# Kernel tuning notes

Hardware: AMD Instinct MI355X
Metric: run time of the kernel (lower is better)

## Reference

```python
import jax, jax.numpy as jnp
import numpy as np

TOP_K = 8
N_GROUP = 8
TOPK_GROUP = 4
ROUTED_SCALING_FACTOR = 2.5
NUM_EXPERTS = 256
HIDDEN = 7168
NUM_TOKENS = 16384


def setup_inputs() -> dict:
    key = jax.random.key(0)
    k1, k2, k3 = jax.random.split(key, 3)
    hidden_states = jax.random.normal(k1, (NUM_TOKENS, HIDDEN), dtype=jnp.float32)
    weight = jax.random.normal(k2, (NUM_EXPERTS, HIDDEN), dtype=jnp.float32) * 0.02
    e_score_correction_bias = jax.random.normal(k3, (NUM_EXPERTS,), dtype=jnp.float32) * 0.1
    return {
        "hidden_states": hidden_states,
        "weight": weight,
        "e_score_correction_bias": e_score_correction_bias,
    }


def reference(hidden_states, weight, e_score_correction_bias):
    # logits: [T, E] = hidden_states @ weight.T  (fp32 gate GEMM)
    logits = jnp.einsum("th,eh->te", hidden_states.astype(jnp.float32), weight)
    scores = jax.nn.sigmoid(logits)                      # [T, E]
    scores_with_bias = scores + e_score_correction_bias  # [T, E]
    T, E = scores_with_bias.shape
    gs = E // N_GROUP  # experts per group

    # group score = sum of top-2 biased scores within each group
    grouped = scores_with_bias.reshape(T, N_GROUP, gs)
    top2, _ = jax.lax.top_k(grouped, 2)                  # [T, G, 2]
    group_scores = top2.sum(axis=-1)                     # [T, G]

    # select topk_group groups, build group mask
    _, group_idx = jax.lax.top_k(group_scores, TOPK_GROUP)  # [T, topk_group]
    rows = jnp.arange(T)[:, None]
    group_mask = jnp.zeros_like(group_scores).at[rows, group_idx].set(1.0)  # [T, G]

    # expand group mask to experts and mask biased scores
    score_mask = jnp.repeat(group_mask, gs, axis=-1)     # [T, E]
    masked_swb = scores_with_bias * score_mask

    # top-k experts over masked biased scores; mask raw sigmoid scores
    _, topk_idx = jax.lax.top_k(masked_swb, TOP_K)       # [T, top_k]
    new_mask = jnp.zeros_like(scores).at[rows, topk_idx].set(1.0)
    sel = scores * new_mask

    # renormalize selected scores and apply routed scaling
    denom = sel.sum(axis=-1, keepdims=True) + 1e-20
    return sel / denom * ROUTED_SCALING_FACTOR
```

## Files before the change

### kernel.cpp

```cpp
#include <hip/hip_runtime.h>
#include <cstdint>
#include <cstddef>

#define HIDDEN 7168
#define NEXP   256
#define KSTEPS (HIDDEN / 32)
#define BM     64
#define ROUTED_SCALE 2.5f


typedef _Float16 half8 __attribute__((ext_vector_type(8)));
typedef float    f32x4 __attribute__((ext_vector_type(4)));

__global__ void convert_w(const float* __restrict__ w, _Float16* __restrict__ ws) {
    int e = blockIdx.x;
    int nt = e >> 4, row = e & 15;
    for (int k = threadIdx.x; k < HIDDEN; k += 256) {
        float x = w[(size_t)e * HIDDEN + k] * 64.0f;
        _Float16 hi = (_Float16)x;
        _Float16 lo = (_Float16)((x - (float)hi) * 4096.0f);
        int s = k >> 5, q = (k >> 3) & 3, j = k & 7;
        size_t off = (size_t)(q * 16 + row) * 8 + j;
        ws[((size_t)((s * 2 + 0) * 16 + nt) << 9) + off] = hi;
        ws[((size_t)((s * 2 + 1) * 16 + nt) << 9) + off] = lo;
    }
}

__global__ __launch_bounds__(512, 2) void gate_kernel(
    const float* __restrict__ hidden,
    const _Float16* __restrict__ wsB,
    const float* __restrict__ bias,
    float* __restrict__ out) {

    __shared__ float lds[BM * 256];

    const int tid    = threadIdx.x;
    const int w      = tid >> 6;
    const int wm     = w >> 2;
    const int wn     = w & 3;
    const int l      = tid & 63;
    const int lane15 = l & 15;
    const int quad   = l >> 4;
    const size_t blockRow = (size_t)blockIdx.x * BM;

    const float* A0 = hidden + (blockRow + wm * 32) * HIDDEN + quad * 8;
    const float* Ap[2];
#pragma unroll
    for (int mt = 0; mt < 2; ++mt)
        Ap[mt] = A0 + (size_t)(mt * 16 + lane15) * HIDDEN;

    const _Float16* Bl = wsB + l * 8;

    f32x4 acc_hh[2][4], acc_c1[2][4];
#pragma unroll
    for (int i = 0; i < 2; ++i)
#pragma unroll
        for (int j = 0; j < 4; ++j) {
            acc_hh[i][j] = (f32x4)0.0f;
            acc_c1[i][j] = (f32x4)0.0f;
        }

    auto loadA = [&](int s, f32x4 (&a)[2][2]) {
#pragma unroll
        for (int mt = 0; mt < 2; ++mt) {
            const float* p = Ap[mt] + s * 32;
            a[mt][0] = *(const f32x4*)(p);
            a[mt][1] = *(const f32x4*)(p + 4);
        }
    };
    auto loadB = [&](int s, half8 (&bh)[4], half8 (&bl)[4]) {
#pragma unroll
        for (int jj = 0; jj < 4; ++jj) {
            int nt = wn * 4 + jj;
            bh[jj] = *(const half8*)(Bl + ((size_t)((s * 2 + 0) * 16 + nt) << 9));
            bl[jj] = *(const half8*)(Bl + ((size_t)((s * 2 + 1) * 16 + nt) << 9));
        }
    };
    auto compute = [&](f32x4 (&a)[2][2], half8 (&bh)[4], half8 (&bl)[4]) {
        half8 ah[2], al[2];
#pragma unroll
        for (int mt = 0; mt < 2; ++mt) {
#pragma unroll
            for (int e = 0; e < 8; ++e) {
                float x = (e < 4) ? a[mt][0][e] : a[mt][1][e - 4];
                _Float16 h = (_Float16)x;
                ah[mt][e] = h;
                al[mt][e] = (_Float16)((x - (float)h) * 4096.0f);
            }
        }
#pragma unroll
        for (int jj = 0; jj < 4; ++jj)
#pragma unroll
            for (int mt = 0; mt < 2; ++mt)
                acc_hh[mt][jj] = __builtin_amdgcn_mfma_f32_16x16x32_f16(ah[mt], bh[jj], acc_hh[mt][jj], 0, 0, 0);
#pragma unroll
        for (int jj = 0; jj < 4; ++jj)
#pragma unroll
            for (int mt = 0; mt < 2; ++mt)
                acc_c1[mt][jj] = __builtin_amdgcn_mfma_f32_16x16x32_f16(al[mt], bh[jj], acc_c1[mt][jj], 0, 0, 0);
#pragma unroll
        for (int jj = 0; jj < 4; ++jj)
#pragma unroll
            for (int mt = 0; mt < 2; ++mt)
                acc_c1[mt][jj] = __builtin_amdgcn_mfma_f32_16x16x32_f16(ah[mt], bl[jj], acc_c1[mt][jj], 0, 0, 0);
    };

    f32x4 a0[2][2], a1[2][2];
    half8 bh0[4], bl0[4], bh1[4], bl1[4];

    loadA(0, a0); loadB(0, bh0, bl0);
    for (int s = 0; s < KSTEPS; s += 2) {
        loadA(s + 1, a1); loadB(s + 1, bh1, bl1);
        compute(a0, bh0, bl0);
        if (s != KSTEPS - 2) { loadA(s + 2, a0); loadB(s + 2, bh0, bl0); }
        compute(a1, bh1, bl1);
    }

#pragma unroll
    for (int mt = 0; mt < 2; ++mt)
#pragma unroll
        for (int jj = 0; jj < 4; ++jj)
#pragma unroll
            for (int r = 0; r < 4; ++r) {
                int row = wm * 32 + mt * 16 + quad * 4 + r;
                int col = wn * 64 + jj * 16 + lane15;
                float logit = (acc_hh[mt][jj][r] + acc_c1[mt][jj][r] * (1.0f / 4096.0f)) * (1.0f / 64.0f);
                lds[row * 256 + col] = logit;
            }
    __syncthreads();

    const int t = tid >> 3;
    const int p = tid & 7;
    float* Lrow = &lds[t * 256];
    const int rot = (t * 4 + p) & 31;

    float t0 = -1e30f, t1 = -1e30f;
    for (int i = 0; i < 32; ++i) {
        int col = p * 32 + ((i + rot) & 31);
        float x  = Lrow[col];
        float sg = 1.0f / (1.0f + expf(-x));
        Lrow[col] = sg;
        float swb = sg + bias[col];
        t1 = fmaxf(t1, fminf(t0, swb));
        t0 = fmaxf(t0, swb);
    }
    float gs = t0 + t1;

    int rank = 0;
#pragma unroll
    for (int m = 1; m < 8; ++m) {
        float ov = __shfl_xor(gs, m);
        int   og = p ^ m;
        rank += (int)((ov > gs) || (ov == gs && og < p));
    }
    bool sel = rank < 4;

    float lv[8], lsr[8]; int li[8];
#pragma unroll
    for (int k = 0; k < 8; ++k) { lv[k] = -1.0f; lsr[k] = 0.0f; li[k] = 1 << 30; }
    for (int i = 0; i < 32; ++i) {
        int col = p * 32 + ((i + rot) & 31);
        float sg  = Lrow[col];
        float swb = sg + bias[col];
        float v = (sel && swb > 0.0f) ? swb : -1.0f;
        if (v > lv[7]) {
            float cv = v, cs = sg; int ci = col;
#pragma unroll
            for (int k = 0; k < 8; ++k) {
                bool sw = cv > lv[k];
                float tv = lv[k], ts = lsr[k]; int ti = li[k];
                lv[k]  = sw ? cv : tv;  lsr[k] = sw ? cs : ts;  li[k] = sw ? ci : ti;
                cv = sw ? tv : cv;  cs = sw ? ts : cs;  ci = sw ? ti : ci;
            }
        }
    }

    unsigned selmask = 0u;
    float denom = 0.0f;
#pragma unroll
    for (int round = 0; round < 8; ++round) {
        float hv = lv[0], hs = lsr[0]; int hidx = li[0];
#pragma unroll
        for (int m = 1; m <= 4; m <<= 1) {
            float ov = __shfl_xor(hv, m);
            float os = __shfl_xor(hs, m);
            int   oi = __shfl_xor(hidx, m);
            bool take = (ov > hv) || (ov == hv && oi < hidx);
            hv = take ? ov : hv;  hs = take ? os : hs;  hidx = take ? oi : hidx;
        }
        if (hv > 0.0f) {
            denom += hs;
            if ((hidx >> 5) == p) selmask |= (1u << (hidx & 31));
        }
        if (li[0] == hidx) {
#pragma unroll
            for (int k = 0; k < 7; ++k) { lv[k] = lv[k + 1]; lsr[k] = lsr[k + 1]; li[k] = li[k + 1]; }
            lv[7] = -1.0f; lsr[7] = 0.0f; li[7] = 1 << 30;
        }
    }

    float inv = ROUTED_SCALE / (denom + 1e-20f);
    float* orow = out + (blockRow + (size_t)t) * NEXP;
    for (int i = 0; i < 32; i += 4) {
        int ii = (i + ((rot & 7) << 2)) & 31;
        int col = p * 32 + ii;
        f32x4 v;
#pragma unroll
        for (int u = 0; u < 4; ++u) {
            float sg = Lrow[col + u];
            bool on = (selmask >> ((col + u) & 31)) & 1u;
            v[u] = on ? sg * inv : 0.0f;
        }
        *(f32x4*)(orow + col) = v;
    }
}

extern "C" void kernel_launch(void* const* d_in, const int* in_sizes, int n_in,
                              void* d_out, int out_size, void* d_ws, size_t ws_size,
                              hipStream_t stream) {
    const float* hidden = (const float*)d_in[0];
    const float* weight = (const float*)d_in[1];
    const float* bias   = (const float*)d_in[2];
    float* out = (float*)d_out;
    _Float16* ws = (_Float16*)d_ws;

    convert_w<<<NEXP, 256, 0, stream>>>(weight, ws);
    gate_kernel<<<16384 / BM, 512, 0, stream>>>(hidden, ws, bias, out);
}
```

Before: 907.4 us.

## Halve gate GEMM row tile to 32 and raise occupancy to four blocks

Shrinks the per-block token tile from 64 to 32 rows, so each wave now computes one 16-row M tile instead of two. The launch bound becomes four blocks per CU, and only half the threads run the routing epilogue. The aim is lower register pressure and more waves in flight to hide global-memory latency on the A/B loads. In exchange, each B (weight) fragment loaded from global memory is reused by half as many MFMAs, so total weight traffic through the caches doubles.

```diff
diff --git a/kernel.cpp b/kernel.cpp
--- a/kernel.cpp
+++ b/kernel.cpp
@@ -5,7 +5,7 @@
 #define HIDDEN 7168
 #define NEXP   256
 #define KSTEPS (HIDDEN / 32)
-#define BM     64
+#define BM     32
 #define ROUTED_SCALE 2.5f
 
 
@@ -26,7 +26,7 @@
     }
 }
 
-__global__ __launch_bounds__(512, 2) void gate_kernel(
+__global__ __launch_bounds__(512, 4) void gate_kernel(
     const float* __restrict__ hidden,
     const _Float16* __restrict__ wsB,
     const float* __restrict__ bias,
@@ -43,30 +43,21 @@
     const int quad   = l >> 4;
     const size_t blockRow = (size_t)blockIdx.x * BM;
 
-    const float* A0 = hidden + (blockRow + wm * 32) * HIDDEN + quad * 8;
-    const float* Ap[2];
-#pragma unroll
-    for (int mt = 0; mt < 2; ++mt)
-        Ap[mt] = A0 + (size_t)(mt * 16 + lane15) * HIDDEN;
+    const float* Ap = hidden + (blockRow + wm * 16 + lane15) * HIDDEN + quad * 8;
 
     const _Float16* Bl = wsB + l * 8;
 
-    f32x4 acc_hh[2][4], acc_c1[2][4];
-#pragma unroll
-    for (int i = 0; i < 2; ++i)
-#pragma unroll
-        for (int j = 0; j < 4; ++j) {
-            acc_hh[i][j] = (f32x4)0.0f;
-            acc_c1[i][j] = (f32x4)0.0f;
-        }
-
-    auto loadA = [&](int s, f32x4 (&a)[2][2]) {
-#pragma unroll
-        for (int mt = 0; mt < 2; ++mt) {
-            const float* p = Ap[mt] + s * 32;
-            a[mt][0] = *(const f32x4*)(p);
-            a[mt][1] = *(const f32x4*)(p + 4);
-        }
+    f32x4 acc_hh[4], acc_c1[4];
+#pragma unroll
+    for (int j = 0; j < 4; ++j) {
+        acc_hh[j] = (f32x4)0.0f;
+        acc_c1[j] = (f32x4)0.0f;
+    }
+
+    auto loadA = [&](int s, f32x4 (&a)[2]) {
+        const float* p = Ap + s * 32;
+        a[0] = *(const f32x4*)(p);
+        a[1] = *(const f32x4*)(p + 4);
     };
     auto loadB = [&](int s, half8 (&bh)[4], half8 (&bl)[4]) {
 #pragma unroll
@@ -76,36 +67,27 @@
             bl[jj] = *(const half8*)(Bl + ((size_t)((s * 2 + 1) * 16 + nt) << 9));
         }
     };
-    auto compute = [&](f32x4 (&a)[2][2], half8 (&bh)[4], half8 (&bl)[4]) {
-        half8 ah[2], al[2];
-#pragma unroll
-        for (int mt = 0; mt < 2; ++mt) {
-#pragma unroll
-            for (int e = 0; e < 8; ++e) {
-                float x = (e < 4) ? a[mt][0][e] : a[mt][1][e - 4];
-                _Float16 h = (_Float16)x;
-                ah[mt][e] = h;
-                al[mt][e] = (_Float16)((x - (float)h) * 4096.0f);
-            }
+    auto compute = [&](f32x4 (&a)[2], half8 (&bh)[4], half8 (&bl)[4]) {
+        half8 ah, al;
+#pragma unroll
+        for (int e = 0; e < 8; ++e) {
+            float x = (e < 4) ? a[0][e] : a[1][e - 4];
+            _Float16 h = (_Float16)x;
+            ah[e] = h;
+            al[e] = (_Float16)((x - (float)h) * 4096.0f);
         }
 #pragma unroll
         for (int jj = 0; jj < 4; ++jj)
-#pragma unroll
-            for (int mt = 0; mt < 2; ++mt)
-                acc_hh[mt][jj] = __builtin_amdgcn_mfma_f32_16x16x32_f16(ah[mt], bh[jj], acc_hh[mt][jj], 0, 0, 0);
+            acc_hh[jj] = __builtin_amdgcn_mfma_f32_16x16x32_f16(ah, bh[jj], acc_hh[jj], 0, 0, 0);
 #pragma unroll
         for (int jj = 0; jj < 4; ++jj)
-#pragma unroll
-            for (int mt = 0; mt < 2; ++mt)
-                acc_c1[mt][jj] = __builtin_amdgcn_mfma_f32_16x16x32_f16(al[mt], bh[jj], acc_c1[mt][jj], 0, 0, 0);
+            acc_c1[jj] = __builtin_amdgcn_mfma_f32_16x16x32_f16(al, bh[jj], acc_c1[jj], 0, 0, 0);
 #pragma unroll
         for (int jj = 0; jj < 4; ++jj)
-#pragma unroll
-            for (int mt = 0; mt < 2; ++mt)
-                acc_c1[mt][jj] = __builtin_amdgcn_mfma_f32_16x16x32_f16(ah[mt], bl[jj], acc_c1[mt][jj], 0, 0, 0);
+            acc_c1[jj] = __builtin_amdgcn_mfma_f32_16x16x32_f16(ah, bl[jj], acc_c1[jj], 0, 0, 0);
     };
 
-    f32x4 a0[2][2], a1[2][2];
+    f32x4 a0[2], a1[2];
     half8 bh0[4], bl0[4], bh1[4], bl1[4];
 
     loadA(0, a0); loadB(0, bh0, bl0);
@@ -117,101 +99,101 @@
     }
 
 #pragma unroll
-    for (int mt = 0; mt < 2; ++mt)
-#pragma unroll
-        for (int jj = 0; jj < 4; ++jj)
-#pragma unroll
-            for (int r = 0; r < 4; ++r) {
-                int row = wm * 32 + mt * 16 + quad * 4 + r;
-                int col = wn * 64 + jj * 16 + lane15;
-                float logit = (acc_hh[mt][jj][r] + acc_c1[mt][jj][r] * (1.0f / 4096.0f)) * (1.0f / 64.0f);
-                lds[row * 256 + col] = logit;
-            }
+    for (int jj = 0; jj < 4; ++jj)
+#pragma unroll
+        for (int r = 0; r < 4; ++r) {
+            int row = wm * 16 + quad * 4 + r;
+            int col = wn * 64 + jj * 16 + lane15;
+            float logit = (acc_hh[jj][r] + acc_c1[jj][r] * (1.0f / 4096.0f)) * (1.0f / 64.0f);
+            lds[row * 256 + col] = logit;
+        }
     __syncthreads();
 
-    const int t = tid >> 3;
-    const int p = tid & 7;
-    float* Lrow = &lds[t * 256];
-    const int rot = (t * 4 + p) & 31;
-
-    float t0 = -1e30f, t1 = -1e30f;
-    for (int i = 0; i < 32; ++i) {
-        int col = p * 32 + ((i + rot) & 31);
-        float x  = Lrow[col];
-        float sg = 1.0f / (1.0f + expf(-x));
-        Lrow[col] = sg;
-        float swb = sg + bias[col];
-        t1 = fmaxf(t1, fminf(t0, swb));
-        t0 = fmaxf(t0, swb);
-    }
-    float gs = t0 + t1;
-
-    int rank = 0;
-#pragma unroll
-    for (int m = 1; m < 8; ++m) {
-        float ov = __shfl_xor(gs, m);
-        int   og = p ^ m;
-        rank += (int)((ov > gs) || (ov == gs && og < p));
-    }
-    bool sel = rank < 4;
-
-    float lv[8], lsr[8]; int li[8];
-#pragma unroll
-    for (int k = 0; k < 8; ++k) { lv[k] = -1.0f; lsr[k] = 0.0f; li[k] = 1 << 30; }
-    for (int i = 0; i < 32; ++i) {
-        int col = p * 32 + ((i + rot) & 31);
-        float sg  = Lrow[col];
-        float swb = sg + bias[col];
-        float v = (sel && swb > 0.0f) ? swb : -1.0f;
-        if (v > lv[7]) {
-            float cv = v, cs = sg; int ci = col;
-#pragma unroll
-            for (int k = 0; k < 8; ++k) {
-                bool sw = cv > lv[k];
-                float tv = lv[k], ts = lsr[k]; int ti = li[k];
-                lv[k]  = sw ? cv : tv;  lsr[k] = sw ? cs : ts;  li[k] = sw ? ci : ti;
-                cv = sw ? tv : cv;  cs = sw ? ts : cs;  ci = sw ? ti : ci;
-            }
-        }
-    }
-
-    unsigned selmask = 0u;
-    float denom = 0.0f;
-#pragma unroll
-    for (int round = 0; round < 8; ++round) {
-        float hv = lv[0], hs = lsr[0]; int hidx = li[0];
-#pragma unroll
-        for (int m = 1; m <= 4; m <<= 1) {
-            float ov = __shfl_xor(hv, m);
-            float os = __shfl_xor(hs, m);
-            int   oi = __shfl_xor(hidx, m);
-            bool take = (ov > hv) || (ov == hv && oi < hidx);
-            hv = take ? ov : hv;  hs = take ? os : hs;  hidx = take ? oi : hidx;
-        }
-        if (hv > 0.0f) {
-            denom += hs;
-            if ((hidx >> 5) == p) selmask |= (1u << (hidx & 31));
-        }
-        if (li[0] == hidx) {
-#pragma unroll
-            for (int k = 0; k < 7; ++k) { lv[k] = lv[k + 1]; lsr[k] = lsr[k + 1]; li[k] = li[k + 1]; }
-            lv[7] = -1.0f; lsr[7] = 0.0f; li[7] = 1 << 30;
-        }
-    }
-
-    float inv = ROUTED_SCALE / (denom + 1e-20f);
-    float* orow = out + (blockRow + (size_t)t) * NEXP;
-    for (int i = 0; i < 32; i += 4) {
-        int ii = (i + ((rot & 7) << 2)) & 31;
-        int col = p * 32 + ii;
-        f32x4 v;
-#pragma unroll
-        for (int u = 0; u < 4; ++u) {
-            float sg = Lrow[col + u];
-            bool on = (selmask >> ((col + u) & 31)) & 1u;
-            v[u] = on ? sg * inv : 0.0f;
-        }
-        *(f32x4*)(orow + col) = v;
+    if (tid < 256) {
+        const int t = tid >> 3;
+        const int p = tid & 7;
+        float* Lrow = &lds[t * 256];
+        const int rot = (t * 4 + p) & 31;
+
+        float t0 = -1e30f, t1 = -1e30f;
+        for (int i = 0; i < 32; ++i) {
+            int col = p * 32 + ((i + rot) & 31);
+            float x  = Lrow[col];
+            float sg = 1.0f / (1.0f + expf(-x));
+            Lrow[col] = sg;
+            float swb = sg + bias[col];
+            t1 = fmaxf(t1, fminf(t0, swb));
+            t0 = fmaxf(t0, swb);
+        }
+        float gs = t0 + t1;
+
+        int rank = 0;
+#pragma unroll
+        for (int m = 1; m < 8; ++m) {
+            float ov = __shfl_xor(gs, m);
+            int   og = p ^ m;
+            rank += (int)((ov > gs) || (ov == gs && og < p));
+        }
+        bool sel = rank < 4;
+
+        float lv[8], lsr[8]; int li[8];
+#pragma unroll
+        for (int k = 0; k < 8; ++k) { lv[k] = -1.0f; lsr[k] = 0.0f; li[k] = 1 << 30; }
+        for (int i = 0; i < 32; ++i) {
+            int col = p * 32 + ((i + rot) & 31);
+            float sg  = Lrow[col];
+            float swb = sg + bias[col];
+            float v = (sel && swb > 0.0f) ? swb : -1.0f;
+            if (v > lv[7]) {
+                float cv = v, cs = sg; int ci = col;
+#pragma unroll
+                for (int k = 0; k < 8; ++k) {
+                    bool sw = cv > lv[k];
+                    float tv = lv[k], ts = lsr[k]; int ti = li[k];
+                    lv[k]  = sw ? cv : tv;  lsr[k] = sw ? cs : ts;  li[k] = sw ? ci : ti;
+                    cv = sw ? tv : cv;  cs = sw ? ts : cs;  ci = sw ? ti : ci;
+                }
+            }
+        }
+
+        unsigned selmask = 0u;
+        float denom = 0.0f;
+#pragma unroll
+        for (int round = 0; round < 8; ++round) {
+            float hv = lv[0], hs = lsr[0]; int hidx = li[0];
+#pragma unroll
+            for (int m = 1; m <= 4; m <<= 1) {
+                float ov = __shfl_xor(hv, m);
+                float os = __shfl_xor(hs, m);
+                int   oi = __shfl_xor(hidx, m);
+                bool take = (ov > hv) || (ov == hv && oi < hidx);
+                hv = take ? ov : hv;  hs = take ? os : hs;  hidx = take ? oi : hidx;
+            }
+            if (hv > 0.0f) {
+                denom += hs;
+                if ((hidx >> 5) == p) selmask |= (1u << (hidx & 31));
+            }
+            if (li[0] == hidx) {
+#pragma unroll
+                for (int k = 0; k < 7; ++k) { lv[k] = lv[k + 1]; lsr[k] = lsr[k + 1]; li[k] = li[k + 1]; }
+                lv[7] = -1.0f; lsr[7] = 0.0f; li[7] = 1 << 30;
+            }
+        }
+
+        float inv = ROUTED_SCALE / (denom + 1e-20f);
+        float* orow = out + (blockRow + (size_t)t) * NEXP;
+        for (int i = 0; i < 32; i += 4) {
+            int ii = (i + ((rot & 7) << 2)) & 31;
+            int col = p * 32 + ii;
+            f32x4 v;
+#pragma unroll
+            for (int u = 0; u < 4; ++u) {
+                float sg = Lrow[col + u];
+                bool on = (selmask >> ((col + u) & 31)) & 1u;
+                v[u] = on ? sg * inv : 0.0f;
+            }
+            *(f32x4*)(orow + col) = v;
+        }
     }
 }
 
```

New measurement: 1.058 ms. +16.6%, slower.

## Split K dimension across two wave groups with LDS reduction

Applied to the files above, without the earlier changes.

Doubles the block to 1024 threads and splits the hidden-dimension loop in half between two groups of 8 waves, each computing a partial GEMM tile. Partial results are combined through LDS in two phases, and only the first 512 threads run the routing epilogue. The aim is more waves in flight to hide memory latency, since the grid has only 256 blocks. The cost is an extra barrier and LDS round trip, plus half the threads sitting idle during the epilogue. The launch bounds of (1024, 4) may also force register pressure or spills.

```diff
diff --git a/kernel.cpp b/kernel.cpp
--- a/kernel.cpp
+++ b/kernel.cpp
@@ -26,7 +26,7 @@
     }
 }
 
-__global__ __launch_bounds__(512, 2) void gate_kernel(
+__global__ __launch_bounds__(1024, 4) void gate_kernel(
     const float* __restrict__ hidden,
     const _Float16* __restrict__ wsB,
     const float* __restrict__ bias,
@@ -36,12 +36,15 @@
 
     const int tid    = threadIdx.x;
     const int w      = tid >> 6;
-    const int wm     = w >> 2;
-    const int wn     = w & 3;
+    const int kh     = w >> 3;
+    const int ws8    = w & 7;
+    const int wm     = ws8 >> 2;
+    const int wn     = ws8 & 3;
     const int l      = tid & 63;
     const int lane15 = l & 15;
     const int quad   = l >> 4;
     const size_t blockRow = (size_t)blockIdx.x * BM;
+    const int sbase = kh * (KSTEPS / 2);
 
     const float* A0 = hidden + (blockRow + wm * 32) * HIDDEN + quad * 8;
     const float* Ap[2];
@@ -108,110 +111,130 @@
     f32x4 a0[2][2], a1[2][2];
     half8 bh0[4], bl0[4], bh1[4], bl1[4];
 
-    loadA(0, a0); loadB(0, bh0, bl0);
-    for (int s = 0; s < KSTEPS; s += 2) {
+    loadA(sbase, a0); loadB(sbase, bh0, bl0);
+    for (int i = 0; i < KSTEPS / 2; i += 2) {
+        int s = sbase + i;
         loadA(s + 1, a1); loadB(s + 1, bh1, bl1);
         compute(a0, bh0, bl0);
-        if (s != KSTEPS - 2) { loadA(s + 2, a0); loadB(s + 2, bh0, bl0); }
+        if (i != KSTEPS / 2 - 2) { loadA(s + 2, a0); loadB(s + 2, bh0, bl0); }
         compute(a1, bh1, bl1);
     }
 
-#pragma unroll
-    for (int mt = 0; mt < 2; ++mt)
-#pragma unroll
-        for (int jj = 0; jj < 4; ++jj)
-#pragma unroll
-            for (int r = 0; r < 4; ++r) {
-                int row = wm * 32 + mt * 16 + quad * 4 + r;
-                int col = wn * 64 + jj * 16 + lane15;
-                float logit = (acc_hh[mt][jj][r] + acc_c1[mt][jj][r] * (1.0f / 4096.0f)) * (1.0f / 64.0f);
-                lds[row * 256 + col] = logit;
-            }
+    if (kh == 0) {
+#pragma unroll
+        for (int mt = 0; mt < 2; ++mt)
+#pragma unroll
+            for (int jj = 0; jj < 4; ++jj)
+#pragma unroll
+                for (int r = 0; r < 4; ++r) {
+                    int row = wm * 32 + mt * 16 + quad * 4 + r;
+                    int col = wn * 64 + jj * 16 + lane15;
+                    lds[row * 256 + col] =
+                        acc_hh[mt][jj][r] + acc_c1[mt][jj][r] * (1.0f / 4096.0f);
+                }
+    }
     __syncthreads();
-
-    const int t = tid >> 3;
-    const int p = tid & 7;
-    float* Lrow = &lds[t * 256];
-    const int rot = (t * 4 + p) & 31;
-
-    float t0 = -1e30f, t1 = -1e30f;
-    for (int i = 0; i < 32; ++i) {
-        int col = p * 32 + ((i + rot) & 31);
-        float x  = Lrow[col];
-        float sg = 1.0f / (1.0f + expf(-x));
-        Lrow[col] = sg;
-        float swb = sg + bias[col];
-        t1 = fmaxf(t1, fminf(t0, swb));
-        t0 = fmaxf(t0, swb);
-    }
-    float gs = t0 + t1;
-
-    int rank = 0;
-#pragma unroll
-    for (int m = 1; m < 8; ++m) {
-        float ov = __shfl_xor(gs, m);
-        int   og = p ^ m;
-        rank += (int)((ov > gs) || (ov == gs && og < p));
-    }
-    bool sel = rank < 4;
-
-    float lv[8], lsr[8]; int li[8];
-#pragma unroll
-    for (int k = 0; k < 8; ++k) { lv[k] = -1.0f; lsr[k] = 0.0f; li[k] = 1 << 30; }
-    for (int i = 0; i < 32; ++i) {
-        int col = p * 32 + ((i + rot) & 31);
-        float sg  = Lrow[col];
-        float swb = sg + bias[col];
-        float v = (sel && swb > 0.0f) ? swb : -1.0f;
-        if (v > lv[7]) {
-            float cv = v, cs = sg; int ci = col;
-#pragma unroll
-            for (int k = 0; k < 8; ++k) {
-                bool sw = cv > lv[k];
-                float tv = lv[k], ts = lsr[k]; int ti = li[k];
-                lv[k]  = sw ? cv : tv;  lsr[k] = sw ? cs : ts;  li[k] = sw ? ci : ti;
-                cv = sw ? tv : cv;  cs = sw ? ts : cs;  ci = sw ? ti : ci;
-            }
-        }
-    }
-
-    unsigned selmask = 0u;
-    float denom = 0.0f;
-#pragma unroll
-    for (int round = 0; round < 8; ++round) {
-        float hv = lv[0], hs = lsr[0]; int hidx = li[0];
-#pragma unroll
-        for (int m = 1; m <= 4; m <<= 1) {
-            float ov = __shfl_xor(hv, m);
-            float os = __shfl_xor(hs, m);
-            int   oi = __shfl_xor(hidx, m);
-            bool take = (ov > hv) || (ov == hv && oi < hidx);
-            hv = take ? ov : hv;  hs = take ? os : hs;  hidx = take ? oi : hidx;
-        }
-        if (hv > 0.0f) {
-            denom += hs;
-            if ((hidx >> 5) == p) selmask |= (1u << (hidx & 31));
-        }
-        if (li[0] == hidx) {
-#pragma unroll
-            for (int k = 0; k < 7; ++k) { lv[k] = lv[k + 1]; lsr[k] = lsr[k + 1]; li[k] = li[k + 1]; }
-            lv[7] = -1.0f; lsr[7] = 0.0f; li[7] = 1 << 30;
-        }
-    }
-
-    float inv = ROUTED_SCALE / (denom + 1e-20f);
-    float* orow = out + (blockRow + (size_t)t) * NEXP;
-    for (int i = 0; i < 32; i += 4) {
-        int ii = (i + ((rot & 7) << 2)) & 31;
-        int col = p * 32 + ii;
-        f32x4 v;
-#pragma unroll
-        for (int u = 0; u < 4; ++u) {
-            float sg = Lrow[col + u];
-            bool on = (selmask >> ((col + u) & 31)) & 1u;
-            v[u] = on ? sg * inv : 0.0f;
-        }
-        *(f32x4*)(orow + col) = v;
+    if (kh == 1) {
+#pragma unroll
+        for (int mt = 0; mt < 2; ++mt)
+#pragma unroll
+            for (int jj = 0; jj < 4; ++jj)
+#pragma unroll
+                for (int r = 0; r < 4; ++r) {
+                    int row = wm * 32 + mt * 16 + quad * 4 + r;
+                    int col = wn * 64 + jj * 16 + lane15;
+                    float v = lds[row * 256 + col] +
+                        (acc_hh[mt][jj][r] + acc_c1[mt][jj][r] * (1.0f / 4096.0f));
+                    lds[row * 256 + col] = v * (1.0f / 64.0f);
+                }
+    }
+    __syncthreads();
+
+    if (tid < 512) {
+        const int t = tid >> 3;
+        const int p = tid & 7;
+        float* Lrow = &lds[t * 256];
+        const int rot = (t * 4 + p) & 31;
+
+        float t0 = -1e30f, t1 = -1e30f;
+        for (int i = 0; i < 32; ++i) {
+            int col = p * 32 + ((i + rot) & 31);
+            float x  = Lrow[col];
+            float sg = 1.0f / (1.0f + expf(-x));
+            Lrow[col] = sg;
+            float swb = sg + bias[col];
+            t1 = fmaxf(t1, fminf(t0, swb));
+            t0 = fmaxf(t0, swb);
+        }
+        float gs = t0 + t1;
+
+        int rank = 0;
+#pragma unroll
+        for (int m = 1; m < 8; ++m) {
+            float ov = __shfl_xor(gs, m);
+            int   og = p ^ m;
+            rank += (int)((ov > gs) || (ov == gs && og < p));
+        }
+        bool sel = rank < 4;
+
+        float lv[8], lsr[8]; int li[8];
+#pragma unroll
+        for (int k = 0; k < 8; ++k) { lv[k] = -1.0f; lsr[k] = 0.0f; li[k] = 1 << 30; }
+        for (int i = 0; i < 32; ++i) {
+            int col = p * 32 + ((i + rot) & 31);
+            float sg  = Lrow[col];
+            float swb = sg + bias[col];
+            float v = (sel && swb > 0.0f) ? swb : -1.0f;
+            if (v > lv[7]) {
+                float cv = v, cs = sg; int ci = col;
+#pragma unroll
+                for (int k = 0; k < 8; ++k) {
+                    bool sw = cv > lv[k];
+                    float tv = lv[k], ts = lsr[k]; int ti = li[k];
+                    lv[k]  = sw ? cv : tv;  lsr[k] = sw ? cs : ts;  li[k] = sw ? ci : ti;
+                    cv = sw ? tv : cv;  cs = sw ? ts : cs;  ci = sw ? ti : ci;
+                }
+            }
+        }
+
+        unsigned selmask = 0u;
+        float denom = 0.0f;
+#pragma unroll
+        for (int round = 0; round < 8; ++round) {
+            float hv = lv[0], hs = lsr[0]; int hidx = li[0];
+#pragma unroll
+            for (int m = 1; m <= 4; m <<= 1) {
+                float ov = __shfl_xor(hv, m);
+                float os = __shfl_xor(hs, m);
+                int   oi = __shfl_xor(hidx, m);
+                bool take = (ov > hv) || (ov == hv && oi < hidx);
+                hv = take ? ov : hv;  hs = take ? os : hs;  hidx = take ? oi : hidx;
+            }
+            if (hv > 0.0f) {
+                denom += hs;
+                if ((hidx >> 5) == p) selmask |= (1u << (hidx & 31));
+            }
+            if (li[0] == hidx) {
+#pragma unroll
+                for (int k = 0; k < 7; ++k) { lv[k] = lv[k + 1]; lsr[k] = lsr[k + 1]; li[k] = li[k + 1]; }
+                lv[7] = -1.0f; lsr[7] = 0.0f; li[7] = 1 << 30;
+            }
+        }
+
+        float inv = ROUTED_SCALE / (denom + 1e-20f);
+        float* orow = out + (blockRow + (size_t)t) * NEXP;
+        for (int i = 0; i < 32; i += 4) {
+            int ii = (i + ((rot & 7) << 2)) & 31;
+            int col = p * 32 + ii;
+            f32x4 v;
+#pragma unroll
+            for (int u = 0; u < 4; ++u) {
+                float sg = Lrow[col + u];
+                bool on = (selmask >> ((col + u) & 31)) & 1u;
+                v[u] = on ? sg * inv : 0.0f;
+            }
+            *(f32x4*)(orow + col) = v;
+        }
     }
 }
 
@@ -225,5 +248,5 @@
     _Float16* ws = (_Float16*)d_ws;
 
     convert_w<<<NEXP, 256, 0, stream>>>(weight, ws);
-    gate_kernel<<<16384 / BM, 512, 0, stream>>>(hidden, ws, bias, out);
+    gate_kernel<<<16384 / BM, 1024, 0, stream>>>(hidden, ws, bias, out);
 }
```

Measured after the change: 2.062 ms. 2.27x slower.

## Split gate GEMM into split-K/N tiles with atomics and separate top-k kernel

Applied to the files above, without the earlier changes.

The fused GEMM+routing kernel is split in two. The GEMM now uses 128-row tiles, splits N into two halves and K into two halves, and accumulates partial logits into the output buffer with atomicAdd after a memset. A separate gate_finish kernel then reads the logits, applies the 1/64 scale, and runs the sigmoid/group top-k routing. This changes the grid shape and parallelism, presumably to improve CU utilization. In exchange it adds a memset, float atomics (non-deterministic summation order), and a full extra round trip of the logits through global memory.

```diff
diff --git a/kernel.cpp b/kernel.cpp
--- a/kernel.cpp
+++ b/kernel.cpp
@@ -4,8 +4,9 @@
 
 #define HIDDEN 7168
 #define NEXP   256
-#define KSTEPS (HIDDEN / 32)
-#define BM     64
+#define KSTEPS 224
+#define KHALF  112
+#define BM     128
 #define ROUTED_SCALE 2.5f
 
 
@@ -26,22 +27,26 @@
     }
 }
 
-__global__ __launch_bounds__(512, 2) void gate_kernel(
+__global__ __launch_bounds__(512, 2) void gemm_kernel(
     const float* __restrict__ hidden,
     const _Float16* __restrict__ wsB,
-    const float* __restrict__ bias,
     float* __restrict__ out) {
 
-    __shared__ float lds[BM * 256];
+    const int bid  = blockIdx.x;
+    const int nhkh = (bid >> 1) & 3;
+    const int nh   = nhkh >> 1;
+    const int kh   = nhkh & 1;
+    const int m    = ((bid >> 3) << 1) | (bid & 1);
 
     const int tid    = threadIdx.x;
     const int w      = tid >> 6;
-    const int wm     = w >> 2;
-    const int wn     = w & 3;
+    const int wm     = w >> 1;
+    const int wn     = w & 1;
     const int l      = tid & 63;
     const int lane15 = l & 15;
     const int quad   = l >> 4;
-    const size_t blockRow = (size_t)blockIdx.x * BM;
+    const size_t blockRow = (size_t)m * BM;
+    const int sbase = kh * KHALF;
 
     const float* A0 = hidden + (blockRow + wm * 32) * HIDDEN + quad * 8;
     const float* Ap[2];
@@ -71,7 +76,7 @@
     auto loadB = [&](int s, half8 (&bh)[4], half8 (&bl)[4]) {
 #pragma unroll
         for (int jj = 0; jj < 4; ++jj) {
-            int nt = wn * 4 + jj;
+            int nt = nh * 8 + wn * 4 + jj;
             bh[jj] = *(const half8*)(Bl + ((size_t)((s * 2 + 0) * 16 + nt) << 9));
             bl[jj] = *(const half8*)(Bl + ((size_t)((s * 2 + 1) * 16 + nt) << 9));
         }
@@ -108,11 +113,12 @@
     f32x4 a0[2][2], a1[2][2];
     half8 bh0[4], bl0[4], bh1[4], bl1[4];
 
-    loadA(0, a0); loadB(0, bh0, bl0);
-    for (int s = 0; s < KSTEPS; s += 2) {
+    loadA(sbase, a0); loadB(sbase, bh0, bl0);
+    for (int i = 0; i < KHALF; i += 2) {
+        int s = sbase + i;
         loadA(s + 1, a1); loadB(s + 1, bh1, bl1);
         compute(a0, bh0, bl0);
-        if (s != KSTEPS - 2) { loadA(s + 2, a0); loadB(s + 2, bh0, bl0); }
+        if (i != KHALF - 2) { loadA(s + 2, a0); loadB(s + 2, bh0, bl0); }
         compute(a1, bh1, bl1);
     }
 
@@ -122,11 +128,30 @@
         for (int jj = 0; jj < 4; ++jj)
 #pragma unroll
             for (int r = 0; r < 4; ++r) {
-                int row = wm * 32 + mt * 16 + quad * 4 + r;
-                int col = wn * 64 + jj * 16 + lane15;
-                float logit = (acc_hh[mt][jj][r] + acc_c1[mt][jj][r] * (1.0f / 4096.0f)) * (1.0f / 64.0f);
-                lds[row * 256 + col] = logit;
+                size_t row = blockRow + wm * 32 + mt * 16 + quad * 4 + r;
+                int col = nh * 128 + wn * 64 + jj * 16 + lane15;
+                float v = acc_hh[mt][jj][r] + acc_c1[mt][jj][r] * (1.0f / 4096.0f);
+                atomicAdd(&out[row * NEXP + col], v);
             }
+}
+
+__global__ __launch_bounds__(256, 4) void gate_finish(
+    const float* __restrict__ bias,
+    float* __restrict__ out) {
+
+    __shared__ float lds[32 * 256];
+
+    const int tid = threadIdx.x;
+    const size_t tbase = (size_t)blockIdx.x * 32;
+
+#pragma unroll
+    for (int i = 0; i < 8; ++i) {
+        int idx = tid + i * 256;
+        int row = idx >> 6, c4 = idx & 63;
+        f32x4 v = *(const f32x4*)(out + (tbase + row) * NEXP + c4 * 4);
+        v = v * (1.0f / 64.0f);
+        *(f32x4*)(&lds[row * 256 + c4 * 4]) = v;
+    }
     __syncthreads();
 
     const int t = tid >> 3;
@@ -200,7 +225,7 @@
     }
 
     float inv = ROUTED_SCALE / (denom + 1e-20f);
-    float* orow = out + (blockRow + (size_t)t) * NEXP;
+    float* orow = out + (tbase + (size_t)t) * NEXP;
     for (int i = 0; i < 32; i += 4) {
         int ii = (i + ((rot & 7) << 2)) & 31;
         int col = p * 32 + ii;
@@ -225,5 +250,7 @@
     _Float16* ws = (_Float16*)d_ws;
 
     convert_w<<<NEXP, 256, 0, stream>>>(weight, ws);
-    gate_kernel<<<16384 / BM, 512, 0, stream>>>(hidden, ws, bias, out);
-}
+    hipMemsetAsync(out, 0, (size_t)16384 * NEXP * sizeof(float), stream);
+    gemm_kernel<<<512, 512, 0, stream>>>(hidden, ws, out);
+    gate_finish<<<512, 256, 0, stream>>>(bias, out);
+}
```

Measured after the change: 939.2 us. 1.04x slower.
